# Kernel tuning notes

Hardware: AMD Instinct MI355X
Metric: run time of the kernel (lower is better)

Reference implementation:

```python
import jax, jax.numpy as jnp
import numpy as np

D = 1024      # d_model
HD = 128      # shared k/v head dim == attn_expert_dim
EA = 8        # attention experts
KA = 2        # attention top-k
EF = 16       # ffn experts
KF = 2        # ffn top-k
FH = 512      # ffn expert hidden dim
MAXP = 64     # max relative positions
B, S = 4, 1024
EPS = 1e-5


def setup_inputs() -> dict:
    key = jax.random.key(0)
    ks = jax.random.split(key, 12)
    r = lambda i, shape, scale=0.02: jax.random.normal(ks[i], shape, jnp.float32) * scale
    return {
        "src": jax.random.normal(ks[0], (B, S, D), jnp.float32),
        "ln1_w": jnp.ones((D,), jnp.float32), "ln1_b": jnp.zeros((D,), jnp.float32),
        "ln2_w": jnp.ones((D,), jnp.float32), "ln2_b": jnp.zeros((D,), jnp.float32),
        "attn_gate_w": r(1, (D, EA)),
        "q_w": r(2, (EA, D, HD)), "q_b": jnp.zeros((EA, HD), jnp.float32),
        "k_w": r(3, (D, HD)), "k_b": jnp.zeros((HD,), jnp.float32),
        "v_w": r(4, (D, HD)), "v_b": jnp.zeros((HD,), jnp.float32),
        "o_w": r(5, (EA, HD, D)), "o_b": jnp.zeros((EA, D), jnp.float32),
        "rel_table": r(6, (2 * MAXP + 1, HD)),
        "ff_gate_w": r(7, (D, EF)),
        "ff_w1": r(8, (EF, D, FH)), "ff_b1": jnp.zeros((EF, FH), jnp.float32),
        "ff_w2": r(9, (EF, FH, D)), "ff_b2": jnp.zeros((EF, D), jnp.float32),
    }


def _layer_norm(x, w, b):
    mu = x.mean(-1, keepdims=True)
    var = ((x - mu) ** 2).mean(-1, keepdims=True)
    return (x - mu) * jax.lax.rsqrt(var + EPS) * w + b


def _topk_gates(logits, k):
    # top-k over router logits, softmax over the selected k, scatter to dense [.., E]
    top_vals, top_idx = jax.lax.top_k(logits, k)
    g = jax.nn.softmax(top_vals, axis=-1)
    onehot = jax.nn.one_hot(top_idx, logits.shape[-1], dtype=logits.dtype)  # [...,k,E]
    return jnp.einsum('...k,...ke->...e', g, onehot)


def _moa(x, gate_w, q_w, q_b, k_w, k_b, v_w, v_b, o_w, o_b, rel_table):
    # Mixture-of-attention: per-expert q/out projections, shared k/v, Shaw rel-pos.
    S_ = x.shape[1]
    gates = _topk_gates(x @ gate_w, KA)                                  # [B,S,EA]
    q = (jnp.einsum('bsd,edh->bseh', x, q_w) + q_b) * (HD ** -0.5)       # [B,S,EA,HD]
    k = x @ k_w + k_b                                                    # [B,S,HD]
    v = x @ v_w + v_b
    scores = jnp.einsum('bqeh,bkh->beqk', q, k)                          # [B,EA,S,S]
    rel_s = jnp.einsum('bqeh,rh->beqr', q, rel_table)                    # [B,EA,S,R]
    pos = jnp.arange(S_)
    rel_idx = jnp.clip(pos[None, :] - pos[:, None], -MAXP, MAXP) + MAXP  # [S,S]
    scores = scores + jnp.take_along_axis(rel_s, rel_idx[None, None], axis=-1)
    p = jax.nn.softmax(scores, axis=-1)
    ctx = jnp.einsum('beqk,bkh->bqeh', p, v)                             # [B,S,EA,HD]
    out = jnp.einsum('bqeh,ehd,bqe->bqd', ctx, o_w, gates)
    return out + jnp.einsum('bqe,ed->bqd', gates, o_b)


def _moe_ffn(x, gate_w, w1, b1, w2, b2):
    gates = _topk_gates(x @ gate_w, KF)                                  # [B,S,EF]
    h = jax.nn.relu(jnp.einsum('bsd,edh->bseh', x, w1) + b1)             # [B,S,EF,FH]
    out = jnp.einsum('bseh,ehd,bse->bsd', h, w2, gates)
    return out + jnp.einsum('bse,ed->bsd', gates, b2)


def reference(src, ln1_w, ln1_b, ln2_w, ln2_b, attn_gate_w, q_w, q_b, k_w, k_b,
              v_w, v_b, o_w, o_b, rel_table, ff_gate_w, ff_w1, ff_b1, ff_w2, ff_b2):
    # pre-LN residual block around MoE attention
    res = src
    xn = _layer_norm(src, ln1_w, ln1_b)
    x = res + _moa(xn, attn_gate_w, q_w, q_b, k_w, k_b, v_w, v_b, o_w, o_b, rel_table)
    # pre-LN residual block around MoE FFN
    res = x
    xn = _layer_norm(x, ln2_w, ln2_b)
    return res + _moe_ffn(xn, ff_gate_w, ff_w1, ff_b1, ff_w2, ff_b2)
```

## Files before the change

### kernel.cpp

```cpp
#include <hip/hip_runtime.h>

#define D 1024
#define HD 128
#define EA 8
#define EF 16
#define FH 512
#define MAXPOS 64
#define RNUM 129
#define RSTRIDE 132
#define SEQ 1024
#define NTOK 4096
#define NPAIR (NTOK * 2)
#define NPAD 8320
#define LN_EPS 1e-5f
#define QSCALE 0.08838834764831845f
#define BSTR 40
#define PROW 2048

typedef __attribute__((ext_vector_type(8))) short bf16x8;
typedef __attribute__((ext_vector_type(4))) float f32x4;
typedef __attribute__((ext_vector_type(8))) unsigned short u16x8;

__device__ inline ushort f2b(float f) {
    union { float f; unsigned u; } v; v.f = f;
    unsigned r = (v.u + 0x7fffu + ((v.u >> 16) & 1u)) >> 16;
    return (ushort)r;
}
__device__ inline float b2f(ushort u) {
    union { unsigned u; float f; } v; v.u = (unsigned)u << 16; return v.f;
}
__device__ inline u16x8 cvt8v(float4 a, float4 b) {
    u16x8 r;
    r[0] = f2b(a.x); r[1] = f2b(a.y); r[2] = f2b(a.z); r[3] = f2b(a.w);
    r[4] = f2b(b.x); r[5] = f2b(b.y); r[6] = f2b(b.z); r[7] = f2b(b.w);
    return r;
}

__device__ inline void mfma_step(const short* Asb, const short* Bsb,
                                 int wr, int wc, int m16, int q, f32x4 (&acc)[2][4]) {
    bf16x8 af[2], bfr[4];
#pragma unroll
    for (int i = 0; i < 2; i++) af[i] = *(const bf16x8*)&Asb[(wr + i * 16 + m16) * BSTR + q * 8];
#pragma unroll
    for (int j = 0; j < 4; j++) bfr[j] = *(const bf16x8*)&Bsb[(wc + j * 16 + m16) * BSTR + q * 8];
#pragma unroll
    for (int i = 0; i < 2; i++)
#pragma unroll
        for (int j = 0; j < 4; j++)
            acc[i][j] = __builtin_amdgcn_mfma_f32_16x16x32_bf16(af[i], bfr[j], acc[i][j], 0, 0, 0);
}

__global__ void ln_kernel(const float* __restrict__ x, const float* __restrict__ w,
                          const float* __restrict__ b, float* __restrict__ y) {
    int row = blockIdx.x;
    const float* xr = x + (size_t)row * D;
    float v[4];
    float s = 0.f, s2 = 0.f;
#pragma unroll
    for (int i = 0; i < 4; i++) {
        v[i] = xr[threadIdx.x + i * 256];
        s += v[i]; s2 += v[i] * v[i];
    }
#pragma unroll
    for (int off = 32; off; off >>= 1) { s += __shfl_down(s, off); s2 += __shfl_down(s2, off); }
    __shared__ float red0[4], red1[4];
    int wave = threadIdx.x >> 6, lane = threadIdx.x & 63;
    if (lane == 0) { red0[wave] = s; red1[wave] = s2; }
    __syncthreads();
    float ts = red0[0] + red0[1] + red0[2] + red0[3];
    float ts2 = red1[0] + red1[1] + red1[2] + red1[3];
    float mu = ts * (1.f / D);
    float var = ts2 * (1.f / D) - mu * mu;
    float inv = rsqrtf(var + LN_EPS);
#pragma unroll
    for (int i = 0; i < 4; i++) {
        int d = threadIdx.x + i * 256;
        y[(size_t)row * D + d] = (v[i] - mu) * inv * w[d] + b[d];
    }
}

template <int E>
__global__ void router_kernel(const float* __restrict__ xn, const float* __restrict__ gw,
                              int* __restrict__ idx, float* __restrict__ gate) {
    int t = blockIdx.x;
    int lane = threadIdx.x;
    float acc[E];
#pragma unroll
    for (int e = 0; e < E; e++) acc[e] = 0.f;
    const float* xr = xn + (size_t)t * D;
    for (int d = lane; d < D; d += 64) {
        float xv = xr[d];
#pragma unroll
        for (int e = 0; e < E; e++) acc[e] += xv * gw[d * E + e];
    }
#pragma unroll
    for (int e = 0; e < E; e++) {
#pragma unroll
        for (int off = 32; off; off >>= 1) acc[e] += __shfl_down(acc[e], off);
    }
    if (lane == 0) {
        float v0 = -1e30f, v1 = -1e30f;
        int i0 = 0, i1 = 0;
#pragma unroll
        for (int e = 0; e < E; e++) {
            float a = acc[e];
            if (a > v0) { v1 = v0; i1 = i0; v0 = a; i0 = e; }
            else if (a > v1) { v1 = a; i1 = e; }
        }
        float g0 = 1.f / (1.f + expf(v1 - v0));
        idx[t * 2] = i0; idx[t * 2 + 1] = i1;
        gate[t * 2] = g0; gate[t * 2 + 1] = 1.f - g0;
    }
}

__global__ void abin_zero(int* __restrict__ meta) {
    if (threadIdx.x < 105) meta[threadIdx.x] = 0;
}
__global__ void abin_count(const int* __restrict__ aidx, int* __restrict__ meta) {
    int i = blockIdx.x * 256 + threadIdx.x;
    if (i < NPAIR) {
        int e = aidx[i];
        int b = (i >> 1) >> 10;
        atomicAdd(&meta[e * 4 + b], 1);
    }
}
__global__ void abin_scan(int* __restrict__ meta) {
    if (threadIdx.x == 0 && blockIdx.x == 0) {
        int s = 0;
        for (int bin = 0; bin < 32; bin++) {
            if ((bin & 3) == 0) meta[96 + (bin >> 2)] = s;
            meta[32 + bin] = s; meta[64 + bin] = s; s += meta[bin];
        }
        meta[96 + 8] = s;
    }
}
__global__ void abin_scatter(const int* __restrict__ aidx, int* __restrict__ meta,
                             int* __restrict__ list, int* __restrict__ inv) {
    int i = blockIdx.x * 256 + threadIdx.x;
    if (i < NPAIR) {
        int e = aidx[i];
        int b = (i >> 1) >> 10;
        int pos = atomicAdd(&meta[64 + e * 4 + b], 1);
        list[pos] = i;
        inv[i] = pos;
    }
}

__global__ void bin_zero(int* __restrict__ meta) {
    if (threadIdx.x < 48) meta[threadIdx.x] = 0;
}
__global__ void bin_count(const int* __restrict__ fidx, int* __restrict__ meta) {
    int i = blockIdx.x * 256 + threadIdx.x;
    if (i < NPAIR) atomicAdd(&meta[fidx[i]], 1);
}
__global__ void bin_scan(int* __restrict__ meta) {
    if (threadIdx.x == 0 && blockIdx.x == 0) {
        int s = 0;
        for (int e = 0; e < EF; e++) { meta[16 + e] = s; meta[32 + e] = s; s += meta[e]; }
    }
}
__global__ void bin_scatter(const int* __restrict__ fidx, int* __restrict__ meta,
                            int* __restrict__ list, int* __restrict__ inv) {
    int i = blockIdx.x * 256 + threadIdx.x;
    if (i < NPAIR) {
        int e = fidx[i];
        int pos = atomicAdd(&meta[32 + e], 1);
        list[pos] = i;
        inv[i] = pos;
    }
}

template <int R, int C>
__global__ void convT_kernel(const float* __restrict__ in, ushort* __restrict__ out) {
    int e = blockIdx.z;
    int r0 = blockIdx.x * 32, c0 = blockIdx.y * 32;
    __shared__ float tile[32][33];
    int tx = threadIdx.x & 31, ty = threadIdx.x >> 5;
    const float* src = in + (size_t)e * R * C;
#pragma unroll
    for (int i = 0; i < 32; i += 8)
        tile[ty + i][tx] = src[(size_t)(r0 + ty + i) * C + c0 + tx];
    __syncthreads();
    ushort* dst = out + (size_t)e * C * R;
#pragma unroll
    for (int i = 0; i < 32; i += 8)
        dst[(size_t)(c0 + ty + i) * R + r0 + tx] = f2b(tile[tx][ty + i]);
}

__global__ void conv_kernel(const float* __restrict__ in, ushort* __restrict__ out, int n) {
    int i = blockIdx.x * 256 + threadIdx.x;
    if (i < n) out[i] = f2b(in[i]);
}

__global__ __launch_bounds__(256) void kv_mfma(
    const float* __restrict__ xn, const ushort* __restrict__ kwt,
    const ushort* __restrict__ vwt, float* __restrict__ kpart, float* __restrict__ vpart) {
    const ushort* W = blockIdx.z ? vwt : kwt;
    float* outp = blockIdx.z ? vpart : kpart;
    int m0 = blockIdx.x * 64;
    int s = blockIdx.y;
    int kbase = s * 256;
    __shared__ __align__(16) short As[2][64 * BSTR];
    __shared__ __align__(16) short Bs[2][128 * BSTR];
    int tid = threadIdx.x, aRow = tid >> 2, aOff = (tid & 3) * 8;
    const float* ap = xn + (size_t)(m0 + aRow) * D + kbase + aOff;
    const ushort* bp0 = W + (size_t)aRow * D + kbase + aOff;
    const ushort* bp1 = bp0 + (size_t)64 * D;
    int w = tid >> 6, lid = tid & 63;
    int wr = (w >> 1) * 32, wc = (w & 1) * 64;
    int m16 = lid & 15, q = lid >> 4;
    f32x4 acc[2][4] = {};
    float4 ra0 = *(const float4*)ap, ra1 = *(const float4*)(ap + 4);
    u16x8 rb0 = *(const u16x8*)bp0, rb1 = *(const u16x8*)bp1;
    *(u16x8*)&As[0][aRow * BSTR + aOff] = cvt8v(ra0, ra1);
    *(u16x8*)&Bs[0][aRow * BSTR + aOff] = rb0;
    *(u16x8*)&Bs[0][(aRow + 64) * BSTR + aOff] = rb1;
    __syncthreads();
    int cur = 0;
    for (int k = 1; k < 8; k++) {
        ra0 = *(const float4*)(ap + k * 32); ra1 = *(const float4*)(ap + k * 32 + 4);
        rb0 = *(const u16x8*)(bp0 + k * 32); rb1 = *(const u16x8*)(bp1 + k * 32);
        mfma_step(As[cur], Bs[cur], wr, wc, m16, q, acc);
        int nxt = cur ^ 1;
        *(u16x8*)&As[nxt][aRow * BSTR + aOff] = cvt8v(ra0, ra1);
        *(u16x8*)&Bs[nxt][aRow * BSTR + aOff] = rb0;
        *(u16x8*)&Bs[nxt][(aRow + 64) * BSTR + aOff] = rb1;
        __syncthreads();
        cur = nxt;
    }
    mfma_step(As[cur], Bs[cur], wr, wc, m16, q, acc);
#pragma unroll
    for (int i = 0; i < 2; i++)
#pragma unroll
        for (int r = 0; r < 4; r++) {
            int m = m0 + wr + i * 16 + q * 4 + r;
#pragma unroll
            for (int j = 0; j < 4; j++)
                outp[((size_t)s * NTOK + m) * HD + wc + j * 16 + m16] = acc[i][j][r];
        }
}

__global__ void kv_reduce(const float* __restrict__ kpart, const float* __restrict__ vpart,
                          const float* __restrict__ kb, const float* __restrict__ vb,
                          float* __restrict__ kbf, float* __restrict__ vbf) {
    int t = blockIdx.x, h = threadIdx.x;
    float ka = kb[h], va = vb[h];
#pragma unroll
    for (int s = 0; s < 4; s++) {
        ka += kpart[((size_t)s * NTOK + t) * HD + h];
        va += vpart[((size_t)s * NTOK + t) * HD + h];
    }
    kbf[(size_t)t * HD + h] = ka;
    vbf[(size_t)t * HD + h] = va;
}

__global__ __launch_bounds__(256) void q_mfma(
    const float* __restrict__ xn, const ushort* __restrict__ qwt,
    const int* __restrict__ meta, const int* __restrict__ list, float* __restrict__ qpart) {
    int e = blockIdx.z;
    int o = meta[96 + e], c = meta[97 + e] - o;
    int m0 = blockIdx.x * 64;
    if (m0 >= c) return;
    int s = blockIdx.y;
    int kbase = s * 256;
    __shared__ __align__(16) short As[2][64 * BSTR];
    __shared__ __align__(16) short Bs[2][128 * BSTR];
    int tid = threadIdx.x, aRow = tid >> 2, aOff = (tid & 3) * 8;
    int ri = o + m0 + aRow; if (ri > NPAIR - 1) ri = NPAIR - 1;
    const float* ap = xn + (size_t)(list[ri] >> 1) * D + kbase + aOff;
    const ushort* bp0 = qwt + (size_t)e * HD * D + (size_t)aRow * D + kbase + aOff;
    const ushort* bp1 = bp0 + (size_t)64 * D;
    int w = tid >> 6, lid = tid & 63;
    int wr = (w >> 1) * 32, wc = (w & 1) * 64;
    int m16 = lid & 15, q = lid >> 4;
    f32x4 acc[2][4] = {};
    float4 ra0 = *(const float4*)ap, ra1 = *(const float4*)(ap + 4);
    u16x8 rb0 = *(const u16x8*)bp0, rb1 = *(const u16x8*)bp1;
    *(u16x8*)&As[0][aRow * BSTR + aOff] = cvt8v(ra0, ra1);
    *(u16x8*)&Bs[0][aRow * BSTR + aOff] = rb0;
    *(u16x8*)&Bs[0][(aRow + 64) * BSTR + aOff] = rb1;
    __syncthreads();
    int cur = 0;
    for (int k = 1; k < 8; k++) {
        ra0 = *(const float4*)(ap + k * 32); ra1 = *(const float4*)(ap + k * 32 + 4);
        rb0 = *(const u16x8*)(bp0 + k * 32); rb1 = *(const u16x8*)(bp1 + k * 32);
        mfma_step(As[cur], Bs[cur], wr, wc, m16, q, acc);
        int nxt = cur ^ 1;
        *(u16x8*)&As[nxt][aRow * BSTR + aOff] = cvt8v(ra0, ra1);
        *(u16x8*)&Bs[nxt][aRow * BSTR + aOff] = rb0;
        *(u16x8*)&Bs[nxt][(aRow + 64) * BSTR + aOff] = rb1;
        __syncthreads();
        cur = nxt;
    }
    mfma_step(As[cur], Bs[cur], wr, wc, m16, q, acc);
#pragma unroll
    for (int i = 0; i < 2; i++)
#pragma unroll
        for (int r = 0; r < 4; r++) {
            int pos = o + m0 + wr + i * 16 + q * 4 + r;
            if (pos < o + c) {
#pragma unroll
                for (int j = 0; j < 4; j++)
                    qpart[((size_t)s * NPAD + pos) * HD + wc + j * 16 + m16] = acc[i][j][r];
            }
        }
}

__global__ void q_reduce(const float* __restrict__ qpart, const float* __restrict__ qb,
                         const int* __restrict__ aidx, const int* __restrict__ list,
                         ushort* __restrict__ Qg) {
    int pos = blockIdx.x, h = threadIdx.x;
    int e = aidx[list[pos]];
    float a = qb[e * HD + h];
#pragma unroll
    for (int s = 0; s < 4; s++) a += qpart[((size_t)s * NPAD + pos) * HD + h];
    Qg[(size_t)pos * HD + h] = f2b(a * QSCALE);
}

__global__ __launch_bounds__(256) void rel_mfma(
    const ushort* __restrict__ Qg, const ushort* __restrict__ relb,
    float* __restrict__ R) {
    int m0 = blockIdx.x * 64;
    int n0 = blockIdx.y * 128;
    __shared__ __align__(16) short As[2][64 * BSTR];
    __shared__ __align__(16) short Bs[2][128 * BSTR];
    int tid = threadIdx.x, aRow = tid >> 2, aOff = (tid & 3) * 8;
    const ushort* ap = Qg + (size_t)(m0 + aRow) * HD + aOff;
    int br0 = n0 + aRow;      if (br0 > RNUM - 1) br0 = RNUM - 1;
    int br1 = n0 + aRow + 64; if (br1 > RNUM - 1) br1 = RNUM - 1;
    const ushort* bp0 = relb + (size_t)br0 * HD + aOff;
    const ushort* bp1 = relb + (size_t)br1 * HD + aOff;
    int w = tid >> 6, lid = tid & 63;
    int wr = (w >> 1) * 32, wc = (w & 1) * 64;
    int m16 = lid & 15, q = lid >> 4;
    f32x4 acc[2][4] = {};
    u16x8 ra = *(const u16x8*)ap;
    u16x8 rb0 = *(const u16x8*)bp0, rb1 = *(const u16x8*)bp1;
    *(u16x8*)&As[0][aRow * BSTR + aOff] = ra;
    *(u16x8*)&Bs[0][aRow * BSTR + aOff] = rb0;
    *(u16x8*)&Bs[0][(aRow + 64) * BSTR + aOff] = rb1;
    __syncthreads();
    int cur = 0;
    for (int k = 1; k < 4; k++) {
        ra = *(const u16x8*)(ap + k * 32);
        rb0 = *(const u16x8*)(bp0 + k * 32); rb1 = *(const u16x8*)(bp1 + k * 32);
        mfma_step(As[cur], Bs[cur], wr, wc, m16, q, acc);
        int nxt = cur ^ 1;
        *(u16x8*)&As[nxt][aRow * BSTR + aOff] = ra;
        *(u16x8*)&Bs[nxt][aRow * BSTR + aOff] = rb0;
        *(u16x8*)&Bs[nxt][(aRow + 64) * BSTR + aOff] = rb1;
        __syncthreads();
        cur = nxt;
    }
    mfma_step(As[cur], Bs[cur], wr, wc, m16, q, acc);
#pragma unroll
    for (int i = 0; i < 2; i++)
#pragma unroll
        for (int r = 0; r < 4; r++) {
            int pos = m0 + wr + i * 16 + q * 4 + r;
#pragma unroll
            for (int j = 0; j < 4; j++) {
                int n = n0 + wc + j * 16 + m16;
                if (n < RNUM) R[(size_t)pos * RSTRIDE + n] = acc[i][j][r];
            }
        }
}

__global__ __launch_bounds__(256) void s_mfma(
    const ushort* __restrict__ Qg, const float* __restrict__ kbf,
    const float* __restrict__ R, const int* __restrict__ meta,
    const int* __restrict__ list, float* __restrict__ S) {
    int bin = blockIdx.z;
    int o = meta[32 + bin], c = meta[bin];
    int m0 = blockIdx.x * 64;
    if (m0 >= c) return;
    int b = bin & 3;
    int n0 = blockIdx.y * 128;
    __shared__ __align__(16) short As[2][64 * BSTR];
    __shared__ __align__(16) short Bs[2][128 * BSTR];
    int tid = threadIdx.x, aRow = tid >> 2, aOff = (tid & 3) * 8;
    const ushort* ap = Qg + (size_t)(o + m0 + aRow) * HD + aOff;
    const float* bp0 = kbf + (size_t)b * SEQ * HD + (size_t)(n0 + aRow) * HD + aOff;
    const float* bp1 = bp0 + (size_t)64 * HD;
    int w = tid >> 6, lid = tid & 63;
    int wr = (w >> 1) * 32, wc = (w & 1) * 64;
    int m16 = lid & 15, q = lid >> 4;
    f32x4 acc[2][4] = {};
    u16x8 ra = *(const u16x8*)ap;
    float4 rb0a = *(const float4*)bp0, rb0b = *(const float4*)(bp0 + 4);
    float4 rb1a = *(const float4*)bp1, rb1b = *(const float4*)(bp1 + 4);
    *(u16x8*)&As[0][aRow * BSTR + aOff] = ra;
    *(u16x8*)&Bs[0][aRow * BSTR + aOff] = cvt8v(rb0a, rb0b);
    *(u16x8*)&Bs[0][(aRow + 64) * BSTR + aOff] = cvt8v(rb1a, rb1b);
    __syncthreads();
    int cur = 0;
    for (int k = 1; k < 4; k++) {
        ra = *(const u16x8*)(ap + k * 32);
        rb0a = *(const float4*)(bp0 + k * 32); rb0b = *(const float4*)(bp0 + k * 32 + 4);
        rb1a = *(const float4*)(bp1 + k * 32); rb1b = *(const float4*)(bp1 + k * 32 + 4);
        mfma_step(As[cur], Bs[cur], wr, wc, m16, q, acc);
        int nxt = cur ^ 1;
        *(u16x8*)&As[nxt][aRow * BSTR + aOff] = ra;
        *(u16x8*)&Bs[nxt][aRow * BSTR + aOff] = cvt8v(rb0a, rb0b);
        *(u16x8*)&Bs[nxt][(aRow + 64) * BSTR + aOff] = cvt8v(rb1a, rb1b);
        __syncthreads();
        cur = nxt;
    }
    mfma_step(As[cur], Bs[cur], wr, wc, m16, q, acc);
#pragma unroll
    for (int i = 0; i < 2; i++)
#pragma unroll
        for (int r = 0; r < 4; r++) {
            int pos = o + m0 + wr + i * 16 + q * 4 + r;
            if (pos < o + c) {
                int qpos = (list[pos] >> 1) & (SEQ - 1);
                const float* Rrow = R + (size_t)pos * RSTRIDE;
                float* sr = S + (size_t)pos * SEQ;
#pragma unroll
                for (int j = 0; j < 4; j++) {
                    int key = n0 + wc + j * 16 + m16;
                    int rix = key - qpos;
                    rix = (rix < -MAXPOS ? -MAXPOS : (rix > MAXPOS ? MAXPOS : rix)) + MAXPOS;
                    sr[key] = acc[i][j][r] + Rrow[rix];
                }
            }
        }
}

__global__ __launch_bounds__(256) void softmax_kernel(float* __restrict__ S) {
    int row = blockIdx.x;
    float4* sr = (float4*)(S + (size_t)row * SEQ);
    float4 v = sr[threadIdx.x];
    float m = fmaxf(fmaxf(v.x, v.y), fmaxf(v.z, v.w));
#pragma unroll
    for (int off = 32; off; off >>= 1) m = fmaxf(m, __shfl_down(m, off));
    __shared__ float red0[4], red1[4];
    int wave = threadIdx.x >> 6, lane = threadIdx.x & 63;
    if (lane == 0) red0[wave] = m;
    __syncthreads();
    m = fmaxf(fmaxf(red0[0], red0[1]), fmaxf(red0[2], red0[3]));
    v.x = __expf(v.x - m); v.y = __expf(v.y - m);
    v.z = __expf(v.z - m); v.w = __expf(v.w - m);
    float s = v.x + v.y + v.z + v.w;
#pragma unroll
    for (int off = 32; off; off >>= 1) s += __shfl_down(s, off);
    if (lane == 0) red1[wave] = s;
    __syncthreads();
    float inv = 1.f / (red1[0] + red1[1] + red1[2] + red1[3]);
    ushort* pr = (ushort*)(S + (size_t)row * SEQ);
    ushort4 p4 = { f2b(v.x * inv), f2b(v.y * inv), f2b(v.z * inv), f2b(v.w * inv) };
    *(ushort4*)(pr + threadIdx.x * 4) = p4;
}

__global__ __launch_bounds__(256) void pv_mfma(
    const ushort* __restrict__ Pb, const ushort* __restrict__ vt16,
    const int* __restrict__ meta, float* __restrict__ ppart) {
    int bin = blockIdx.z;
    int o = meta[32 + bin], c = meta[bin];
    int m0 = blockIdx.x * 64;
    if (m0 >= c) return;
    int b = bin & 3;
    int s = blockIdx.y;
    int kbase = s * 256;
    __shared__ __align__(16) short As[2][64 * BSTR];
    __shared__ __align__(16) short Bs[2][128 * BSTR];
    int tid = threadIdx.x, aRow = tid >> 2, aOff = (tid & 3) * 8;
    const ushort* ap = Pb + (size_t)(o + m0 + aRow) * PROW + kbase + aOff;
    const ushort* bp0 = vt16 + (size_t)b * HD * SEQ + (size_t)aRow * SEQ + kbase + aOff;
    const ushort* bp1 = bp0 + (size_t)64 * SEQ;
    int w = tid >> 6, lid = tid & 63;
    int wr = (w >> 1) * 32, wc = (w & 1) * 64;
    int m16 = lid & 15, q = lid >> 4;
    f32x4 acc[2][4] = {};
    u16x8 ra = *(const u16x8*)ap;
    u16x8 rb0 = *(const u16x8*)bp0, rb1 = *(const u16x8*)bp1;
    *(u16x8*)&As[0][aRow * BSTR + aOff] = ra;
    *(u16x8*)&Bs[0][aRow * BSTR + aOff] = rb0;
    *(u16x8*)&Bs[0][(aRow + 64) * BSTR + aOff] = rb1;
    __syncthreads();
    int cur = 0;
    for (int k = 1; k < 8; k++) {
        ra = *(const u16x8*)(ap + k * 32);
        rb0 = *(const u16x8*)(bp0 + k * 32); rb1 = *(const u16x8*)(bp1 + k * 32);
        mfma_step(As[cur], Bs[cur], wr, wc, m16, q, acc);
        int nxt = cur ^ 1;
        *(u16x8*)&As[nxt][aRow * BSTR + aOff] = ra;
        *(u16x8*)&Bs[nxt][aRow * BSTR + aOff] = rb0;
        *(u16x8*)&Bs[nxt][(aRow + 64) * BSTR + aOff] = rb1;
        __syncthreads();
        cur = nxt;
    }
    mfma_step(As[cur], Bs[cur], wr, wc, m16, q, acc);
#pragma unroll
    for (int i = 0; i < 2; i++)
#pragma unroll
        for (int r = 0; r < 4; r++) {
            int pos = o + m0 + wr + i * 16 + q * 4 + r;
            if (pos < o + c) {
#pragma unroll
                for (int j = 0; j < 4; j++)
                    ppart[((size_t)s * NPAD + pos) * HD + wc + j * 16 + m16] = acc[i][j][r];
            }
        }
}

__global__ void pv_reduce(const float* __restrict__ ppart, const float* __restrict__ aga,
                          const int* __restrict__ list, float* __restrict__ ctxf) {
    int pos = blockIdx.x, h = threadIdx.x;
    float g = aga[list[pos]];
    float a = 0.f;
#pragma unroll
    for (int s = 0; s < 4; s++) a += ppart[((size_t)s * NPAD + pos) * HD + h];
    ctxf[(size_t)pos * HD + h] = a * g;
}

__global__ __launch_bounds__(256) void o_mfma(
    const float* __restrict__ ctxf, const ushort* __restrict__ owt,
    const int* __restrict__ meta, ushort* __restrict__ Ofb) {
    int e = blockIdx.z;
    int o = meta[96 + e], c = meta[97 + e] - o;
    int m0 = blockIdx.x * 64;
    if (m0 >= c) return;
    int n0 = blockIdx.y * 128;
    __shared__ __align__(16) short As[2][64 * BSTR];
    __shared__ __align__(16) short Bs[2][128 * BSTR];
    int tid = threadIdx.x, aRow = tid >> 2, aOff = (tid & 3) * 8;
    const float* ap = ctxf + (size_t)(o + m0 + aRow) * HD + aOff;
    const ushort* bp0 = owt + (size_t)e * D * HD + (size_t)(n0 + aRow) * HD + aOff;
    const ushort* bp1 = bp0 + (size_t)64 * HD;
    int w = tid >> 6, lid = tid & 63;
    int wr = (w >> 1) * 32, wc = (w & 1) * 64;
    int m16 = lid & 15, q = lid >> 4;
    f32x4 acc[2][4] = {};
    float4 ra0 = *(const float4*)ap, ra1 = *(const float4*)(ap + 4);
    u16x8 rb0 = *(const u16x8*)bp0, rb1 = *(const u16x8*)bp1;
    *(u16x8*)&As[0][aRow * BSTR + aOff] = cvt8v(ra0, ra1);
    *(u16x8*)&Bs[0][aRow * BSTR + aOff] = rb0;
    *(u16x8*)&Bs[0][(aRow + 64) * BSTR + aOff] = rb1;
    __syncthreads();
    int cur = 0;
    for (int k = 1; k < 4; k++) {
        ra0 = *(const float4*)(ap + k * 32); ra1 = *(const float4*)(ap + k * 32 + 4);
        rb0 = *(const u16x8*)(bp0 + k * 32); rb1 = *(const u16x8*)(bp1 + k * 32);
        mfma_step(As[cur], Bs[cur], wr, wc, m16, q, acc);
        int nxt = cur ^ 1;
        *(u16x8*)&As[nxt][aRow * BSTR + aOff] = cvt8v(ra0, ra1);
        *(u16x8*)&Bs[nxt][aRow * BSTR + aOff] = rb0;
        *(u16x8*)&Bs[nxt][(aRow + 64) * BSTR + aOff] = rb1;
        __syncthreads();
        cur = nxt;
    }
    mfma_step(As[cur], Bs[cur], wr, wc, m16, q, acc);
#pragma unroll
    for (int i = 0; i < 2; i++)
#pragma unroll
        for (int r = 0; r < 4; r++) {
            int pos = o + m0 + wr + i * 16 + q * 4 + r;
            if (pos < o + c) {
#pragma unroll
                for (int j = 0; j < 4; j++)
                    Ofb[(size_t)pos * D + n0 + wc + j * 16 + m16] = f2b(acc[i][j][r]);
            }
        }
}

__global__ void attn_combine(const float* __restrict__ src, const float* __restrict__ ob,
                             const int* __restrict__ aidx, const float* __restrict__ aga,
                             const int* __restrict__ ainv, const ushort* __restrict__ Ofb,
                             float* __restrict__ x1) {
    int t = blockIdx.x, tid = threadIdx.x;
    int e0 = aidx[t * 2], e1 = aidx[t * 2 + 1];
    float g0 = aga[t * 2], g1 = aga[t * 2 + 1];
    int p0 = ainv[t * 2], p1 = ainv[t * 2 + 1];
#pragma unroll
    for (int i = 0; i < 4; i++) {
        int d = tid + i * 256;
        x1[(size_t)t * D + d] = src[(size_t)t * D + d]
                              + g0 * ob[e0 * D + d] + g1 * ob[e1 * D + d]
                              + b2f(Ofb[(size_t)p0 * D + d]) + b2f(Ofb[(size_t)p1 * D + d]);
    }
}

__global__ __launch_bounds__(256) void ffn_mfma1(
    const float* __restrict__ xn2, const ushort* __restrict__ w1t,
    const float* __restrict__ b1, const int* __restrict__ meta,
    const int* __restrict__ list, const float* __restrict__ fga,
    ushort* __restrict__ Hb) {
    int e = blockIdx.z;
    int o = meta[16 + e], c = meta[e];
    int m0 = blockIdx.x * 64;
    if (m0 >= c) return;
    int n0 = blockIdx.y * 128;
    __shared__ __align__(16) short As[2][64 * BSTR];
    __shared__ __align__(16) short Bs[2][128 * BSTR];
    int tid = threadIdx.x, aRow = tid >> 2, aOff = (tid & 3) * 8;
    int ri = o + m0 + aRow; if (ri > NPAIR - 1) ri = NPAIR - 1;
    const float* ap = xn2 + (size_t)(list[ri] >> 1) * D + aOff;
    const ushort* bp0 = w1t + ((size_t)e * FH + n0 + aRow) * D + aOff;
    const ushort* bp1 = bp0 + (size_t)64 * D;
    int w = tid >> 6, lid = tid & 63;
    int wr = (w >> 1) * 32, wc = (w & 1) * 64;
    int m16 = lid & 15, q = lid >> 4;
    f32x4 acc[2][4] = {};
    float4 ra0 = *(const float4*)ap, ra1 = *(const float4*)(ap + 4);
    u16x8 rb0 = *(const u16x8*)bp0, rb1 = *(const u16x8*)bp1;
    *(u16x8*)&As[0][aRow * BSTR + aOff] = cvt8v(ra0, ra1);
    *(u16x8*)&Bs[0][aRow * BSTR + aOff] = rb0;
    *(u16x8*)&Bs[0][(aRow + 64) * BSTR + aOff] = rb1;
    __syncthreads();
    int cur = 0;
    for (int k = 1; k < 32; k++) {
        ra0 = *(const float4*)(ap + k * 32); ra1 = *(const float4*)(ap + k * 32 + 4);
        rb0 = *(const u16x8*)(bp0 + k * 32); rb1 = *(const u16x8*)(bp1 + k * 32);
        mfma_step(As[cur], Bs[cur], wr, wc, m16, q, acc);
        int nxt = cur ^ 1;
        *(u16x8*)&As[nxt][aRow * BSTR + aOff] = cvt8v(ra0, ra1);
        *(u16x8*)&Bs[nxt][aRow * BSTR + aOff] = rb0;
        *(u16x8*)&Bs[nxt][(aRow + 64) * BSTR + aOff] = rb1;
        __syncthreads();
        cur = nxt;
    }
    mfma_step(As[cur], Bs[cur], wr, wc, m16, q, acc);
#pragma unroll
    for (int i = 0; i < 2; i++)
#pragma unroll
        for (int r = 0; r < 4; r++) {
            int pos = o + m0 + wr + i * 16 + q * 4 + r;
            if (pos < o + c) {
                float g = fga[list[pos]];
#pragma unroll
                for (int j = 0; j < 4; j++) {
                    int n = n0 + wc + j * 16 + m16;
                    Hb[(size_t)pos * FH + n] = f2b(g * fmaxf(acc[i][j][r] + b1[e * FH + n], 0.f));
                }
            }
        }
}

__global__ __launch_bounds__(256) void ffn_mfma2(
    const ushort* __restrict__ Hb, const ushort* __restrict__ w2t,
    const int* __restrict__ meta, ushort* __restrict__ Of2b) {
    int e = blockIdx.z;
    int o = meta[16 + e], c = meta[e];
    int m0 = blockIdx.x * 64;
    if (m0 >= c) return;
    int n0 = blockIdx.y * 128;
    __shared__ __align__(16) short As[2][64 * BSTR];
    __shared__ __align__(16) short Bs[2][128 * BSTR];
    int tid = threadIdx.x, aRow = tid >> 2, aOff = (tid & 3) * 8;
    const ushort* ap = Hb + (size_t)(o + m0 + aRow) * FH + aOff;
    const ushort* bp0 = w2t + ((size_t)e * D + n0 + aRow) * FH + aOff;
    const ushort* bp1 = bp0 + (size_t)64 * FH;
    int w = tid >> 6, lid = tid & 63;
    int wr = (w >> 1) * 32, wc = (w & 1) * 64;
    int m16 = lid & 15, q = lid >> 4;
    f32x4 acc[2][4] = {};
    u16x8 ra = *(const u16x8*)ap;
    u16x8 rb0 = *(const u16x8*)bp0, rb1 = *(const u16x8*)bp1;
    *(u16x8*)&As[0][aRow * BSTR + aOff] = ra;
    *(u16x8*)&Bs[0][aRow * BSTR + aOff] = rb0;
    *(u16x8*)&Bs[0][(aRow + 64) * BSTR + aOff] = rb1;
    __syncthreads();
    int cur = 0;
    for (int k = 1; k < 16; k++) {
        ra = *(const u16x8*)(ap + k * 32);
        rb0 = *(const u16x8*)(bp0 + k * 32); rb1 = *(const u16x8*)(bp1 + k * 32);
        mfma_step(As[cur], Bs[cur], wr, wc, m16, q, acc);
        int nxt = cur ^ 1;
        *(u16x8*)&As[nxt][aRow * BSTR + aOff] = ra;
        *(u16x8*)&Bs[nxt][aRow * BSTR + aOff] = rb0;
        *(u16x8*)&Bs[nxt][(aRow + 64) * BSTR + aOff] = rb1;
        __syncthreads();
        cur = nxt;
    }
    mfma_step(As[cur], Bs[cur], wr, wc, m16, q, acc);
#pragma unroll
    for (int i = 0; i < 2; i++)
#pragma unroll
        for (int r = 0; r < 4; r++) {
            int pos = o + m0 + wr + i * 16 + q * 4 + r;
            if (pos < o + c) {
#pragma unroll
                for (int j = 0; j < 4; j++)
                    Of2b[(size_t)pos * D + n0 + wc + j * 16 + m16] = f2b(acc[i][j][r]);
            }
        }
}

__global__ void ffn_combine(const float* __restrict__ x1, const float* __restrict__ b2,
                            const int* __restrict__ fidx, const float* __restrict__ fga,
                            const int* __restrict__ finv, const ushort* __restrict__ Of2b,
                            float* __restrict__ out) {
    int t = blockIdx.x, tid = threadIdx.x;
    int e0 = fidx[t * 2], e1 = fidx[t * 2 + 1];
    float g0 = fga[t * 2], g1 = fga[t * 2 + 1];
    int p0 = finv[t * 2], p1 = finv[t * 2 + 1];
#pragma unroll
    for (int i = 0; i < 4; i++) {
        int d = tid + i * 256;
        out[(size_t)t * D + d] = x1[(size_t)t * D + d]
                               + g0 * b2[e0 * D + d] + g1 * b2[e1 * D + d]
                               + b2f(Of2b[(size_t)p0 * D + d]) + b2f(Of2b[(size_t)p1 * D + d]);
    }
}

extern "C" void kernel_launch(void* const* d_in, const int* in_sizes, int n_in,
                              void* d_out, int out_size, void* d_ws, size_t ws_size,
                              hipStream_t stream) {
    const float* src   = (const float*)d_in[0];
    const float* ln1_w = (const float*)d_in[1];
    const float* ln1_b = (const float*)d_in[2];
    const float* ln2_w = (const float*)d_in[3];
    const float* ln2_b = (const float*)d_in[4];
    const float* agw   = (const float*)d_in[5];
    const float* qw    = (const float*)d_in[6];
    const float* qb    = (const float*)d_in[7];
    const float* kw    = (const float*)d_in[8];
    const float* kb    = (const float*)d_in[9];
    const float* vw    = (const float*)d_in[10];
    const float* vb    = (const float*)d_in[11];
    const float* ow    = (const float*)d_in[12];
    const float* ob    = (const float*)d_in[13];
    const float* rel   = (const float*)d_in[14];
    const float* fgw   = (const float*)d_in[15];
    const float* w1    = (const float*)d_in[16];
    const float* b1    = (const float*)d_in[17];
    const float* w2    = (const float*)d_in[18];
    const float* b2    = (const float*)d_in[19];
    float* out = (float*)d_out;

    char* p = (char*)d_ws;
    float* xn1  = (float*)p; p += (size_t)NTOK * D * 4;
    float* x1   = (float*)p; p += (size_t)NTOK * D * 4;
    char*  sreg = p;         p += (size_t)NPAD * SEQ * 4;
    float*  Sbuf = (float*)sreg;
    ushort* Pb   = (ushort*)sreg;
    ushort* Ofb  = (ushort*)sreg;
    ushort* w1t  = (ushort*)sreg;
    ushort* w2t  = (ushort*)(sreg + (size_t)16777216);
    char*  reg  = p;         p += (size_t)NPAD * 128 * 6 + (size_t)NPAIR * RSTRIDE * 4;
    float*  ctxf = (float*)reg;
    ushort* Qg   = (ushort*)(reg + (size_t)NPAD * 128 * 4);
    float*  Rbuf = (float*)(reg + (size_t)NPAD * 128 * 6);
    ushort* Hb   = (ushort*)reg;
    char*  arena = p;        p += (size_t)4 * NPAD * 128 * 4;
    float*  kpart = (float*)arena;
    float*  vpart = (float*)(arena + (size_t)4 * NTOK * HD * 4);
    float*  qpart = (float*)arena;
    float*  ppart = (float*)arena;
    ushort* Of2b  = (ushort*)arena;
    float* kbf  = (float*)p; p += (size_t)NTOK * HD * 4;
    float* vbf  = (float*)p; p += (size_t)NTOK * HD * 4;
    ushort* vt16 = (ushort*)p; p += (size_t)NTOK * HD * 2;
    ushort* kwt = (ushort*)p; p += (size_t)HD * D * 2;
    ushort* vwt = (ushort*)p; p += (size_t)HD * D * 2;
    ushort* qwt = (ushort*)p; p += (size_t)EA * HD * D * 2;
    ushort* owt = (ushort*)p; p += (size_t)EA * D * HD * 2;
    ushort* relb = (ushort*)p; p += (size_t)RNUM * HD * 2 + 256;
    int*   aidx = (int*)p;   p += NPAIR * 4;
    float* aga  = (float*)p; p += NPAIR * 4;
    int*   fidx = (int*)p;   p += NPAIR * 4;
    float* fga  = (float*)p; p += NPAIR * 4;
    int*   ameta = (int*)p;  p += 128 * 4;
    int*   alist = (int*)p;  p += NPAIR * 4;
    int*   ainv = (int*)p;   p += NPAIR * 4;
    int*   fmeta = (int*)p;  p += 64 * 4;
    int*   flist = (int*)p;  p += NPAIR * 4;
    int*   finv = (int*)p;   p += NPAIR * 4;
    float* xn2 = xn1;

    ln_kernel<<<NTOK, 256, 0, stream>>>(src, ln1_w, ln1_b, xn1);
    router_kernel<EA><<<NTOK, 64, 0, stream>>>(xn1, agw, aidx, aga);
    abin_zero<<<1, 128, 0, stream>>>(ameta);
    abin_count<<<NPAIR / 256, 256, 0, stream>>>(aidx, ameta);
    abin_scan<<<1, 64, 0, stream>>>(ameta);
    abin_scatter<<<NPAIR / 256, 256, 0, stream>>>(aidx, ameta, alist, ainv);
    convT_kernel<1024, 128><<<dim3(32, 4, 1), 256, 0, stream>>>(kw, kwt);
    convT_kernel<1024, 128><<<dim3(32, 4, 1), 256, 0, stream>>>(vw, vwt);
    convT_kernel<1024, 128><<<dim3(32, 4, EA), 256, 0, stream>>>(qw, qwt);
    convT_kernel<128, 1024><<<dim3(4, 32, EA), 256, 0, stream>>>(ow, owt);
    conv_kernel<<<(RNUM * HD + 255) / 256, 256, 0, stream>>>(rel, relb, RNUM * HD);
    kv_mfma<<<dim3(64, 4, 2), 256, 0, stream>>>(xn1, kwt, vwt, kpart, vpart);
    kv_reduce<<<NTOK, 128, 0, stream>>>(kpart, vpart, kb, vb, kbf, vbf);
    convT_kernel<1024, 128><<<dim3(32, 4, 4), 256, 0, stream>>>(vbf, vt16);
    q_mfma<<<dim3(40, 4, EA), 256, 0, stream>>>(xn1, qwt, ameta, alist, qpart);
    q_reduce<<<NPAIR, 128, 0, stream>>>(qpart, qb, aidx, alist, Qg);
    rel_mfma<<<dim3(NPAIR / 64, 2), 256, 0, stream>>>(Qg, relb, Rbuf);
    s_mfma<<<dim3(12, 8, 32), 256, 0, stream>>>(Qg, kbf, Rbuf, ameta, alist, Sbuf);
    softmax_kernel<<<NPAIR, 256, 0, stream>>>(Sbuf);
    pv_mfma<<<dim3(12, 4, 32), 256, 0, stream>>>(Pb, vt16, ameta, ppart);
    pv_reduce<<<NPAIR, 128, 0, stream>>>(ppart, aga, alist, ctxf);
    o_mfma<<<dim3(40, 8, EA), 256, 0, stream>>>(ctxf, owt, ameta, Ofb);
    attn_combine<<<NTOK, 256, 0, stream>>>(src, ob, aidx, aga, ainv, Ofb, x1);

    ln_kernel<<<NTOK, 256, 0, stream>>>(x1, ln2_w, ln2_b, xn2);
    router_kernel<EF><<<NTOK, 64, 0, stream>>>(xn2, fgw, fidx, fga);
    bin_zero<<<1, 64, 0, stream>>>(fmeta);
    bin_count<<<NPAIR / 256, 256, 0, stream>>>(fidx, fmeta);
    bin_scan<<<1, 64, 0, stream>>>(fmeta);
    bin_scatter<<<NPAIR / 256, 256, 0, stream>>>(fidx, fmeta, flist, finv);
    convT_kernel<1024, 512><<<dim3(32, 16, EF), 256, 0, stream>>>(w1, w1t);
    convT_kernel<512, 1024><<<dim3(16, 32, EF), 256, 0, stream>>>(w2, w2t);
    ffn_mfma1<<<dim3(20, 4, EF), 256, 0, stream>>>(xn2, w1t, b1, fmeta, flist, fga, Hb);
    ffn_mfma2<<<dim3(20, 8, EF), 256, 0, stream>>>(Hb, w2t, fmeta, Of2b);
    ffn_combine<<<NTOK, 256, 0, stream>>>(x1, b2, fidx, fga, finv, Of2b, out);
}
```

Baseline: 516.8 us.

## Stage GEMM tiles with global_load_lds and feed bf16 activations from producers

```diff
diff --git a/kernel.cpp b/kernel.cpp
--- a/kernel.cpp
+++ b/kernel.cpp
@@ -14,7 +14,7 @@
 #define NPAD 8320
 #define LN_EPS 1e-5f
 #define QSCALE 0.08838834764831845f
-#define BSTR 40
+#define BSTR 32
 #define PROW 2048
 
 typedef __attribute__((ext_vector_type(8))) short bf16x8;
@@ -29,11 +29,10 @@
 __device__ inline float b2f(ushort u) {
     union { unsigned u; float f; } v; v.u = (unsigned)u << 16; return v.f;
 }
-__device__ inline u16x8 cvt8v(float4 a, float4 b) {
-    u16x8 r;
-    r[0] = f2b(a.x); r[1] = f2b(a.y); r[2] = f2b(a.z); r[3] = f2b(a.w);
-    r[4] = f2b(b.x); r[5] = f2b(b.y); r[6] = f2b(b.z); r[7] = f2b(b.w);
-    return r;
+
+__device__ __forceinline__ void gll(const void* g, void* l) {
+    __builtin_amdgcn_global_load_lds((const __attribute__((address_space(1))) void*)g,
+                                     (__attribute__((address_space(3))) void*)l, 16, 0, 0);
 }
 
 __device__ inline void mfma_step(const short* Asb, const short* Bsb,
@@ -51,7 +50,8 @@
 }
 
 __global__ void ln_kernel(const float* __restrict__ x, const float* __restrict__ w,
-                          const float* __restrict__ b, float* __restrict__ y) {
+                          const float* __restrict__ b, float* __restrict__ y,
+                          ushort* __restrict__ yb) {
     int row = blockIdx.x;
     const float* xr = x + (size_t)row * D;
     float v[4];
@@ -75,7 +75,9 @@
 #pragma unroll
     for (int i = 0; i < 4; i++) {
         int d = threadIdx.x + i * 256;
-        y[(size_t)row * D + d] = (v[i] - mu) * inv * w[d] + b[d];
+        float o = (v[i] - mu) * inv * w[d] + b[d];
+        y[(size_t)row * D + d] = o;
+        yb[(size_t)row * D + d] = f2b(o);
     }
 }
 
@@ -192,8 +194,9 @@
     if (i < n) out[i] = f2b(in[i]);
 }
 
+
 __global__ __launch_bounds__(256) void kv_mfma(
-    const float* __restrict__ xn, const ushort* __restrict__ kwt,
+    const ushort* __restrict__ xnb, const ushort* __restrict__ kwt,
     const ushort* __restrict__ vwt, float* __restrict__ kpart, float* __restrict__ vpart) {
     const ushort* W = blockIdx.z ? vwt : kwt;
     float* outp = blockIdx.z ? vpart : kpart;
@@ -202,29 +205,23 @@
     int kbase = s * 256;
     __shared__ __align__(16) short As[2][64 * BSTR];
     __shared__ __align__(16) short Bs[2][128 * BSTR];
-    int tid = threadIdx.x, aRow = tid >> 2, aOff = (tid & 3) * 8;
-    const float* ap = xn + (size_t)(m0 + aRow) * D + kbase + aOff;
-    const ushort* bp0 = W + (size_t)aRow * D + kbase + aOff;
-    const ushort* bp1 = bp0 + (size_t)64 * D;
-    int w = tid >> 6, lid = tid & 63;
+    int tid = threadIdx.x, w = tid >> 6, lane = tid & 63;
+    int sr = lane >> 2, sc = (lane & 3) * 8;
+    const ushort* ap = xnb + (size_t)(m0 + w * 16 + sr) * D + kbase + sc;
+    const ushort* bp0 = W + (size_t)(w * 32 + sr) * D + kbase + sc;
+    const ushort* bp1 = bp0 + (size_t)16 * D;
     int wr = (w >> 1) * 32, wc = (w & 1) * 64;
-    int m16 = lid & 15, q = lid >> 4;
+    int m16 = lane & 15, q = lane >> 4;
     f32x4 acc[2][4] = {};
-    float4 ra0 = *(const float4*)ap, ra1 = *(const float4*)(ap + 4);
-    u16x8 rb0 = *(const u16x8*)bp0, rb1 = *(const u16x8*)bp1;
-    *(u16x8*)&As[0][aRow * BSTR + aOff] = cvt8v(ra0, ra1);
-    *(u16x8*)&Bs[0][aRow * BSTR + aOff] = rb0;
-    *(u16x8*)&Bs[0][(aRow + 64) * BSTR + aOff] = rb1;
+    gll(ap, &As[0][w * 512]); gll(bp0, &Bs[0][w * 1024]); gll(bp1, &Bs[0][w * 1024 + 512]);
     __syncthreads();
     int cur = 0;
     for (int k = 1; k < 8; k++) {
-        ra0 = *(const float4*)(ap + k * 32); ra1 = *(const float4*)(ap + k * 32 + 4);
-        rb0 = *(const u16x8*)(bp0 + k * 32); rb1 = *(const u16x8*)(bp1 + k * 32);
+        int nxt = cur ^ 1;
+        gll(ap + k * 32, &As[nxt][w * 512]);
+        gll(bp0 + k * 32, &Bs[nxt][w * 1024]);
+        gll(bp1 + k * 32, &Bs[nxt][w * 1024 + 512]);
         mfma_step(As[cur], Bs[cur], wr, wc, m16, q, acc);
-        int nxt = cur ^ 1;
-        *(u16x8*)&As[nxt][aRow * BSTR + aOff] = cvt8v(ra0, ra1);
-        *(u16x8*)&Bs[nxt][aRow * BSTR + aOff] = rb0;
-        *(u16x8*)&Bs[nxt][(aRow + 64) * BSTR + aOff] = rb1;
         __syncthreads();
         cur = nxt;
     }
@@ -242,7 +239,7 @@
 
 __global__ void kv_reduce(const float* __restrict__ kpart, const float* __restrict__ vpart,
                           const float* __restrict__ kb, const float* __restrict__ vb,
-                          float* __restrict__ kbf, float* __restrict__ vbf) {
+                          ushort* __restrict__ kb16, float* __restrict__ vbf) {
     int t = blockIdx.x, h = threadIdx.x;
     float ka = kb[h], va = vb[h];
 #pragma unroll
@@ -250,12 +247,12 @@
         ka += kpart[((size_t)s * NTOK + t) * HD + h];
         va += vpart[((size_t)s * NTOK + t) * HD + h];
     }
-    kbf[(size_t)t * HD + h] = ka;
+    kb16[(size_t)t * HD + h] = f2b(ka);
     vbf[(size_t)t * HD + h] = va;
 }
 
 __global__ __launch_bounds__(256) void q_mfma(
-    const float* __restrict__ xn, const ushort* __restrict__ qwt,
+    const ushort* __restrict__ xnb, const ushort* __restrict__ qwt,
     const int* __restrict__ meta, const int* __restrict__ list, float* __restrict__ qpart) {
     int e = blockIdx.z;
     int o = meta[96 + e], c = meta[97 + e] - o;
@@ -265,30 +262,24 @@
     int kbase = s * 256;
     __shared__ __align__(16) short As[2][64 * BSTR];
     __shared__ __align__(16) short Bs[2][128 * BSTR];
-    int tid = threadIdx.x, aRow = tid >> 2, aOff = (tid & 3) * 8;
-    int ri = o + m0 + aRow; if (ri > NPAIR - 1) ri = NPAIR - 1;
-    const float* ap = xn + (size_t)(list[ri] >> 1) * D + kbase + aOff;
-    const ushort* bp0 = qwt + (size_t)e * HD * D + (size_t)aRow * D + kbase + aOff;
-    const ushort* bp1 = bp0 + (size_t)64 * D;
-    int w = tid >> 6, lid = tid & 63;
+    int tid = threadIdx.x, w = tid >> 6, lane = tid & 63;
+    int sr = lane >> 2, sc = (lane & 3) * 8;
+    int ri = o + m0 + w * 16 + sr; if (ri > NPAIR - 1) ri = NPAIR - 1;
+    const ushort* ap = xnb + (size_t)(list[ri] >> 1) * D + kbase + sc;
+    const ushort* bp0 = qwt + (size_t)e * HD * D + (size_t)(w * 32 + sr) * D + kbase + sc;
+    const ushort* bp1 = bp0 + (size_t)16 * D;
     int wr = (w >> 1) * 32, wc = (w & 1) * 64;
-    int m16 = lid & 15, q = lid >> 4;
+    int m16 = lane & 15, q = lane >> 4;
     f32x4 acc[2][4] = {};
-    float4 ra0 = *(const float4*)ap, ra1 = *(const float4*)(ap + 4);
-    u16x8 rb0 = *(const u16x8*)bp0, rb1 = *(const u16x8*)bp1;
-    *(u16x8*)&As[0][aRow * BSTR + aOff] = cvt8v(ra0, ra1);
-    *(u16x8*)&Bs[0][aRow * BSTR + aOff] = rb0;
-    *(u16x8*)&Bs[0][(aRow + 64) * BSTR + aOff] = rb1;
+    gll(ap, &As[0][w * 512]); gll(bp0, &Bs[0][w * 1024]); gll(bp1, &Bs[0][w * 1024 + 512]);
     __syncthreads();
     int cur = 0;
     for (int k = 1; k < 8; k++) {
-        ra0 = *(const float4*)(ap + k * 32); ra1 = *(const float4*)(ap + k * 32 + 4);
-        rb0 = *(const u16x8*)(bp0 + k * 32); rb1 = *(const u16x8*)(bp1 + k * 32);
+        int nxt = cur ^ 1;
+        gll(ap + k * 32, &As[nxt][w * 512]);
+        gll(bp0 + k * 32, &Bs[nxt][w * 1024]);
+        gll(bp1 + k * 32, &Bs[nxt][w * 1024 + 512]);
         mfma_step(As[cur], Bs[cur], wr, wc, m16, q, acc);
-        int nxt = cur ^ 1;
-        *(u16x8*)&As[nxt][aRow * BSTR + aOff] = cvt8v(ra0, ra1);
-        *(u16x8*)&Bs[nxt][aRow * BSTR + aOff] = rb0;
-        *(u16x8*)&Bs[nxt][(aRow + 64) * BSTR + aOff] = rb1;
         __syncthreads();
         cur = nxt;
     }
@@ -324,31 +315,25 @@
     int n0 = blockIdx.y * 128;
     __shared__ __align__(16) short As[2][64 * BSTR];
     __shared__ __align__(16) short Bs[2][128 * BSTR];
-    int tid = threadIdx.x, aRow = tid >> 2, aOff = (tid & 3) * 8;
-    const ushort* ap = Qg + (size_t)(m0 + aRow) * HD + aOff;
-    int br0 = n0 + aRow;      if (br0 > RNUM - 1) br0 = RNUM - 1;
-    int br1 = n0 + aRow + 64; if (br1 > RNUM - 1) br1 = RNUM - 1;
-    const ushort* bp0 = relb + (size_t)br0 * HD + aOff;
-    const ushort* bp1 = relb + (size_t)br1 * HD + aOff;
-    int w = tid >> 6, lid = tid & 63;
+    int tid = threadIdx.x, w = tid >> 6, lane = tid & 63;
+    int sr = lane >> 2, sc = (lane & 3) * 8;
+    const ushort* ap = Qg + (size_t)(m0 + w * 16 + sr) * HD + sc;
+    int r0 = n0 + w * 32 + sr;      if (r0 > RNUM - 1) r0 = RNUM - 1;
+    int r1 = n0 + w * 32 + 16 + sr; if (r1 > RNUM - 1) r1 = RNUM - 1;
+    const ushort* bp0 = relb + (size_t)r0 * HD + sc;
+    const ushort* bp1 = relb + (size_t)r1 * HD + sc;
     int wr = (w >> 1) * 32, wc = (w & 1) * 64;
-    int m16 = lid & 15, q = lid >> 4;
+    int m16 = lane & 15, q = lane >> 4;
     f32x4 acc[2][4] = {};
-    u16x8 ra = *(const u16x8*)ap;
-    u16x8 rb0 = *(const u16x8*)bp0, rb1 = *(const u16x8*)bp1;
-    *(u16x8*)&As[0][aRow * BSTR + aOff] = ra;
-    *(u16x8*)&Bs[0][aRow * BSTR + aOff] = rb0;
-    *(u16x8*)&Bs[0][(aRow + 64) * BSTR + aOff] = rb1;
+    gll(ap, &As[0][w * 512]); gll(bp0, &Bs[0][w * 1024]); gll(bp1, &Bs[0][w * 1024 + 512]);
     __syncthreads();
     int cur = 0;
     for (int k = 1; k < 4; k++) {
-        ra = *(const u16x8*)(ap + k * 32);
-        rb0 = *(const u16x8*)(bp0 + k * 32); rb1 = *(const u16x8*)(bp1 + k * 32);
+        int nxt = cur ^ 1;
+        gll(ap + k * 32, &As[nxt][w * 512]);
+        gll(bp0 + k * 32, &Bs[nxt][w * 1024]);
+        gll(bp1 + k * 32, &Bs[nxt][w * 1024 + 512]);
         mfma_step(As[cur], Bs[cur], wr, wc, m16, q, acc);
-        int nxt = cur ^ 1;
-        *(u16x8*)&As[nxt][aRow * BSTR + aOff] = ra;
-        *(u16x8*)&Bs[nxt][aRow * BSTR + aOff] = rb0;
-        *(u16x8*)&Bs[nxt][(aRow + 64) * BSTR + aOff] = rb1;
         __syncthreads();
         cur = nxt;
     }
@@ -367,7 +352,7 @@
 }
 
 __global__ __launch_bounds__(256) void s_mfma(
-    const ushort* __restrict__ Qg, const float* __restrict__ kbf,
+    const ushort* __restrict__ Qg, const ushort* __restrict__ kb16,
     const float* __restrict__ R, const int* __restrict__ meta,
     const int* __restrict__ list, float* __restrict__ S) {
     int bin = blockIdx.z;
@@ -378,31 +363,23 @@
     int n0 = blockIdx.y * 128;
     __shared__ __align__(16) short As[2][64 * BSTR];
     __shared__ __align__(16) short Bs[2][128 * BSTR];
-    int tid = threadIdx.x, aRow = tid >> 2, aOff = (tid & 3) * 8;
-    const ushort* ap = Qg + (size_t)(o + m0 + aRow) * HD + aOff;
-    const float* bp0 = kbf + (size_t)b * SEQ * HD + (size_t)(n0 + aRow) * HD + aOff;
-    const float* bp1 = bp0 + (size_t)64 * HD;
-    int w = tid >> 6, lid = tid & 63;
+    int tid = threadIdx.x, w = tid >> 6, lane = tid & 63;
+    int sr = lane >> 2, sc = (lane & 3) * 8;
+    const ushort* ap = Qg + (size_t)(o + m0 + w * 16 + sr) * HD + sc;
+    const ushort* bp0 = kb16 + (size_t)b * SEQ * HD + (size_t)(n0 + w * 32 + sr) * HD + sc;
+    const ushort* bp1 = bp0 + (size_t)16 * HD;
     int wr = (w >> 1) * 32, wc = (w & 1) * 64;
-    int m16 = lid & 15, q = lid >> 4;
+    int m16 = lane & 15, q = lane >> 4;
     f32x4 acc[2][4] = {};
-    u16x8 ra = *(const u16x8*)ap;
-    float4 rb0a = *(const float4*)bp0, rb0b = *(const float4*)(bp0 + 4);
-    float4 rb1a = *(const float4*)bp1, rb1b = *(const float4*)(bp1 + 4);
-    *(u16x8*)&As[0][aRow * BSTR + aOff] = ra;
-    *(u16x8*)&Bs[0][aRow * BSTR + aOff] = cvt8v(rb0a, rb0b);
-    *(u16x8*)&Bs[0][(aRow + 64) * BSTR + aOff] = cvt8v(rb1a, rb1b);
+    gll(ap, &As[0][w * 512]); gll(bp0, &Bs[0][w * 1024]); gll(bp1, &Bs[0][w * 1024 + 512]);
     __syncthreads();
     int cur = 0;
     for (int k = 1; k < 4; k++) {
-        ra = *(const u16x8*)(ap + k * 32);
-        rb0a = *(const float4*)(bp0 + k * 32); rb0b = *(const float4*)(bp0 + k * 32 + 4);
-        rb1a = *(const float4*)(bp1 + k * 32); rb1b = *(const float4*)(bp1 + k * 32 + 4);
+        int nxt = cur ^ 1;
+        gll(ap + k * 32, &As[nxt][w * 512]);
+        gll(bp0 + k * 32, &Bs[nxt][w * 1024]);
+        gll(bp1 + k * 32, &Bs[nxt][w * 1024 + 512]);
         mfma_step(As[cur], Bs[cur], wr, wc, m16, q, acc);
-        int nxt = cur ^ 1;
-        *(u16x8*)&As[nxt][aRow * BSTR + aOff] = ra;
-        *(u16x8*)&Bs[nxt][aRow * BSTR + aOff] = cvt8v(rb0a, rb0b);
-        *(u16x8*)&Bs[nxt][(aRow + 64) * BSTR + aOff] = cvt8v(rb1a, rb1b);
         __syncthreads();
         cur = nxt;
     }
@@ -415,13 +392,13 @@
             if (pos < o + c) {
                 int qpos = (list[pos] >> 1) & (SEQ - 1);
                 const float* Rrow = R + (size_t)pos * RSTRIDE;
-                float* sr = S + (size_t)pos * SEQ;
+                float* sr_ = S + (size_t)pos * SEQ;
 #pragma unroll
                 for (int j = 0; j < 4; j++) {
                     int key = n0 + wc + j * 16 + m16;
                     int rix = key - qpos;
                     rix = (rix < -MAXPOS ? -MAXPOS : (rix > MAXPOS ? MAXPOS : rix)) + MAXPOS;
-                    sr[key] = acc[i][j][r] + Rrow[rix];
+                    sr_[key] = acc[i][j][r] + Rrow[rix];
                 }
             }
         }
@@ -464,29 +441,23 @@
     int kbase = s * 256;
     __shared__ __align__(16) short As[2][64 * BSTR];
     __shared__ __align__(16) short Bs[2][128 * BSTR];
-    int tid = threadIdx.x, aRow = tid >> 2, aOff = (tid & 3) * 8;
-    const ushort* ap = Pb + (size_t)(o + m0 + aRow) * PROW + kbase + aOff;
-    const ushort* bp0 = vt16 + (size_t)b * HD * SEQ + (size_t)aRow * SEQ + kbase + aOff;
-    const ushort* bp1 = bp0 + (size_t)64 * SEQ;
-    int w = tid >> 6, lid = tid & 63;
+    int tid = threadIdx.x, w = tid >> 6, lane = tid & 63;
+    int sr = lane >> 2, sc = (lane & 3) * 8;
+    const ushort* ap = Pb + (size_t)(o + m0 + w * 16 + sr) * PROW + kbase + sc;
+    const ushort* bp0 = vt16 + (size_t)b * HD * SEQ + (size_t)(w * 32 + sr) * SEQ + kbase + sc;
+    const ushort* bp1 = bp0 + (size_t)16 * SEQ;
     int wr = (w >> 1) * 32, wc = (w & 1) * 64;
-    int m16 = lid & 15, q = lid >> 4;
+    int m16 = lane & 15, q = lane >> 4;
     f32x4 acc[2][4] = {};
-    u16x8 ra = *(const u16x8*)ap;
-    u16x8 rb0 = *(const u16x8*)bp0, rb1 = *(const u16x8*)bp1;
-    *(u16x8*)&As[0][aRow * BSTR + aOff] = ra;
-    *(u16x8*)&Bs[0][aRow * BSTR + aOff] = rb0;
-    *(u16x8*)&Bs[0][(aRow + 64) * BSTR + aOff] = rb1;
+    gll(ap, &As[0][w * 512]); gll(bp0, &Bs[0][w * 1024]); gll(bp1, &Bs[0][w * 1024 + 512]);
     __syncthreads();
     int cur = 0;
     for (int k = 1; k < 8; k++) {
-        ra = *(const u16x8*)(ap + k * 32);
-        rb0 = *(const u16x8*)(bp0 + k * 32); rb1 = *(const u16x8*)(bp1 + k * 32);
+        int nxt = cur ^ 1;
+        gll(ap + k * 32, &As[nxt][w * 512]);
+        gll(bp0 + k * 32, &Bs[nxt][w * 1024]);
+        gll(bp1 + k * 32, &Bs[nxt][w * 1024 + 512]);
         mfma_step(As[cur], Bs[cur], wr, wc, m16, q, acc);
-        int nxt = cur ^ 1;
-        *(u16x8*)&As[nxt][aRow * BSTR + aOff] = ra;
-        *(u16x8*)&Bs[nxt][aRow * BSTR + aOff] = rb0;
-        *(u16x8*)&Bs[nxt][(aRow + 64) * BSTR + aOff] = rb1;
         __syncthreads();
         cur = nxt;
     }
@@ -505,17 +476,17 @@
 }
 
 __global__ void pv_reduce(const float* __restrict__ ppart, const float* __restrict__ aga,
-                          const int* __restrict__ list, float* __restrict__ ctxf) {
+                          const int* __restrict__ list, ushort* __restrict__ ctx16) {
     int pos = blockIdx.x, h = threadIdx.x;
     float g = aga[list[pos]];
     float a = 0.f;
 #pragma unroll
     for (int s = 0; s < 4; s++) a += ppart[((size_t)s * NPAD + pos) * HD + h];
-    ctxf[(size_t)pos * HD + h] = a * g;
+    ctx16[(size_t)pos * HD + h] = f2b(a * g);
 }
 
 __global__ __launch_bounds__(256) void o_mfma(
-    const float* __restrict__ ctxf, const ushort* __restrict__ owt,
+    const ushort* __restrict__ ctx16, const ushort* __restrict__ owt,
     const int* __restrict__ meta, ushort* __restrict__ Ofb) {
     int e = blockIdx.z;
     int o = meta[96 + e], c = meta[97 + e] - o;
@@ -524,29 +495,23 @@
     int n0 = blockIdx.y * 128;
     __shared__ __align__(16) short As[2][64 * BSTR];
     __shared__ __align__(16) short Bs[2][128 * BSTR];
-    int tid = threadIdx.x, aRow = tid >> 2, aOff = (tid & 3) * 8;
-    const float* ap = ctxf + (size_t)(o + m0 + aRow) * HD + aOff;
-    const ushort* bp0 = owt + (size_t)e * D * HD + (size_t)(n0 + aRow) * HD + aOff;
-    const ushort* bp1 = bp0 + (size_t)64 * HD;
-    int w = tid >> 6, lid = tid & 63;
+    int tid = threadIdx.x, w = tid >> 6, lane = tid & 63;
+    int sr = lane >> 2, sc = (lane & 3) * 8;
+    const ushort* ap = ctx16 + (size_t)(o + m0 + w * 16 + sr) * HD + sc;
+    const ushort* bp0 = owt + (size_t)e * D * HD + (size_t)(n0 + w * 32 + sr) * HD + sc;
+    const ushort* bp1 = bp0 + (size_t)16 * HD;
     int wr = (w >> 1) * 32, wc = (w & 1) * 64;
-    int m16 = lid & 15, q = lid >> 4;
+    int m16 = lane & 15, q = lane >> 4;
     f32x4 acc[2][4] = {};
-    float4 ra0 = *(const float4*)ap, ra1 = *(const float4*)(ap + 4);
-    u16x8 rb0 = *(const u16x8*)bp0, rb1 = *(const u16x8*)bp1;
-    *(u16x8*)&As[0][aRow * BSTR + aOff] = cvt8v(ra0, ra1);
-    *(u16x8*)&Bs[0][aRow * BSTR + aOff] = rb0;
-    *(u16x8*)&Bs[0][(aRow + 64) * BSTR + aOff] = rb1;
+    gll(ap, &As[0][w * 512]); gll(bp0, &Bs[0][w * 1024]); gll(bp1, &Bs[0][w * 1024 + 512]);
     __syncthreads();
     int cur = 0;
     for (int k = 1; k < 4; k++) {
-        ra0 = *(const float4*)(ap + k * 32); ra1 = *(const float4*)(ap + k * 32 + 4);
-        rb0 = *(const u16x8*)(bp0 + k * 32); rb1 = *(const u16x8*)(bp1 + k * 32);
+        int nxt = cur ^ 1;
+        gll(ap + k * 32, &As[nxt][w * 512]);
+        gll(bp0 + k * 32, &Bs[nxt][w * 1024]);
+        gll(bp1 + k * 32, &Bs[nxt][w * 1024 + 512]);
         mfma_step(As[cur], Bs[cur], wr, wc, m16, q, acc);
-        int nxt = cur ^ 1;
-        *(u16x8*)&As[nxt][aRow * BSTR + aOff] = cvt8v(ra0, ra1);
-        *(u16x8*)&Bs[nxt][aRow * BSTR + aOff] = rb0;
-        *(u16x8*)&Bs[nxt][(aRow + 64) * BSTR + aOff] = rb1;
         __syncthreads();
         cur = nxt;
     }
@@ -582,7 +547,7 @@
 }
 
 __global__ __launch_bounds__(256) void ffn_mfma1(
-    const float* __restrict__ xn2, const ushort* __restrict__ w1t,
+    const ushort* __restrict__ xnb2, const ushort* __restrict__ w1t,
     const float* __restrict__ b1, const int* __restrict__ meta,
     const int* __restrict__ list, const float* __restrict__ fga,
     ushort* __restrict__ Hb) {
@@ -593,30 +558,24 @@
     int n0 = blockIdx.y * 128;
     __shared__ __align__(16) short As[2][64 * BSTR];
     __shared__ __align__(16) short Bs[2][128 * BSTR];
-    int tid = threadIdx.x, aRow = tid >> 2, aOff = (tid & 3) * 8;
-    int ri = o + m0 + aRow; if (ri > NPAIR - 1) ri = NPAIR - 1;
-    const float* ap = xn2 + (size_t)(list[ri] >> 1) * D + aOff;
-    const ushort* bp0 = w1t + ((size_t)e * FH + n0 + aRow) * D + aOff;
-    const ushort* bp1 = bp0 + (size_t)64 * D;
-    int w = tid >> 6, lid = tid & 63;
+    int tid = threadIdx.x, w = tid >> 6, lane = tid & 63;
+    int sr = lane >> 2, sc = (lane & 3) * 8;
+    int ri = o + m0 + w * 16 + sr; if (ri > NPAIR - 1) ri = NPAIR - 1;
+    const ushort* ap = xnb2 + (size_t)(list[ri] >> 1) * D + sc;
+    const ushort* bp0 = w1t + ((size_t)e * FH + n0 + w * 32 + sr) * D + sc;
+    const ushort* bp1 = bp0 + (size_t)16 * D;
     int wr = (w >> 1) * 32, wc = (w & 1) * 64;
-    int m16 = lid & 15, q = lid >> 4;
+    int m16 = lane & 15, q = lane >> 4;
     f32x4 acc[2][4] = {};
-    float4 ra0 = *(const float4*)ap, ra1 = *(const float4*)(ap + 4);
-    u16x8 rb0 = *(const u16x8*)bp0, rb1 = *(const u16x8*)bp1;
-    *(u16x8*)&As[0][aRow * BSTR + aOff] = cvt8v(ra0, ra1);
-    *(u16x8*)&Bs[0][aRow * BSTR + aOff] = rb0;
-    *(u16x8*)&Bs[0][(aRow + 64) * BSTR + aOff] = rb1;
+    gll(ap, &As[0][w * 512]); gll(bp0, &Bs[0][w * 1024]); gll(bp1, &Bs[0][w * 1024 + 512]);
     __syncthreads();
     int cur = 0;
     for (int k = 1; k < 32; k++) {
-        ra0 = *(const float4*)(ap + k * 32); ra1 = *(const float4*)(ap + k * 32 + 4);
-        rb0 = *(const u16x8*)(bp0 + k * 32); rb1 = *(const u16x8*)(bp1 + k * 32);
+        int nxt = cur ^ 1;
+        gll(ap + k * 32, &As[nxt][w * 512]);
+        gll(bp0 + k * 32, &Bs[nxt][w * 1024]);
+        gll(bp1 + k * 32, &Bs[nxt][w * 1024 + 512]);
         mfma_step(As[cur], Bs[cur], wr, wc, m16, q, acc);
-        int nxt = cur ^ 1;
-        *(u16x8*)&As[nxt][aRow * BSTR + aOff] = cvt8v(ra0, ra1);
-        *(u16x8*)&Bs[nxt][aRow * BSTR + aOff] = rb0;
-        *(u16x8*)&Bs[nxt][(aRow + 64) * BSTR + aOff] = rb1;
         __syncthreads();
         cur = nxt;
     }
@@ -647,29 +606,23 @@
     int n0 = blockIdx.y * 128;
     __shared__ __align__(16) short As[2][64 * BSTR];
     __shared__ __align__(16) short Bs[2][128 * BSTR];
-    int tid = threadIdx.x, aRow = tid >> 2, aOff = (tid & 3) * 8;
-    const ushort* ap = Hb + (size_t)(o + m0 + aRow) * FH + aOff;
-    const ushort* bp0 = w2t + ((size_t)e * D + n0 + aRow) * FH + aOff;
-    const ushort* bp1 = bp0 + (size_t)64 * FH;
-    int w = tid >> 6, lid = tid & 63;
+    int tid = threadIdx.x, w = tid >> 6, lane = tid & 63;
+    int sr = lane >> 2, sc = (lane & 3) * 8;
+    const ushort* ap = Hb + (size_t)(o + m0 + w * 16 + sr) * FH + sc;
+    const ushort* bp0 = w2t + ((size_t)e * D + n0 + w * 32 + sr) * FH + sc;
+    const ushort* bp1 = bp0 + (size_t)16 * FH;
     int wr = (w >> 1) * 32, wc = (w & 1) * 64;
-    int m16 = lid & 15, q = lid >> 4;
+    int m16 = lane & 15, q = lane >> 4;
     f32x4 acc[2][4] = {};
-    u16x8 ra = *(const u16x8*)ap;
-    u16x8 rb0 = *(const u16x8*)bp0, rb1 = *(const u16x8*)bp1;
-    *(u16x8*)&As[0][aRow * BSTR + aOff] = ra;
-    *(u16x8*)&Bs[0][aRow * BSTR + aOff] = rb0;
-    *(u16x8*)&Bs[0][(aRow + 64) * BSTR + aOff] = rb1;
+    gll(ap, &As[0][w * 512]); gll(bp0, &Bs[0][w * 1024]); gll(bp1, &Bs[0][w * 1024 + 512]);
     __syncthreads();
     int cur = 0;
     for (int k = 1; k < 16; k++) {
-        ra = *(const u16x8*)(ap + k * 32);
-        rb0 = *(const u16x8*)(bp0 + k * 32); rb1 = *(const u16x8*)(bp1 + k * 32);
+        int nxt = cur ^ 1;
+        gll(ap + k * 32, &As[nxt][w * 512]);
+        gll(bp0 + k * 32, &Bs[nxt][w * 1024]);
+        gll(bp1 + k * 32, &Bs[nxt][w * 1024 + 512]);
         mfma_step(As[cur], Bs[cur], wr, wc, m16, q, acc);
-        int nxt = cur ^ 1;
-        *(u16x8*)&As[nxt][aRow * BSTR + aOff] = ra;
-        *(u16x8*)&Bs[nxt][aRow * BSTR + aOff] = rb0;
-        *(u16x8*)&Bs[nxt][(aRow + 64) * BSTR + aOff] = rb1;
         __syncthreads();
         cur = nxt;
     }
@@ -739,7 +692,7 @@
     ushort* w1t  = (ushort*)sreg;
     ushort* w2t  = (ushort*)(sreg + (size_t)16777216);
     char*  reg  = p;         p += (size_t)NPAD * 128 * 6 + (size_t)NPAIR * RSTRIDE * 4;
-    float*  ctxf = (float*)reg;
+    ushort* ctx16 = (ushort*)reg;
     ushort* Qg   = (ushort*)(reg + (size_t)NPAD * 128 * 4);
     float*  Rbuf = (float*)(reg + (size_t)NPAD * 128 * 6);
     ushort* Hb   = (ushort*)reg;
@@ -749,7 +702,7 @@
     float*  qpart = (float*)arena;
     float*  ppart = (float*)arena;
     ushort* Of2b  = (ushort*)arena;
-    float* kbf  = (float*)p; p += (size_t)NTOK * HD * 4;
+    ushort* kb16 = (ushort*)p; p += (size_t)NTOK * HD * 2;
     float* vbf  = (float*)p; p += (size_t)NTOK * HD * 4;
     ushort* vt16 = (ushort*)p; p += (size_t)NTOK * HD * 2;
     ushort* kwt = (ushort*)p; p += (size_t)HD * D * 2;
@@ -767,9 +720,10 @@
     int*   fmeta = (int*)p;  p += 64 * 4;
     int*   flist = (int*)p;  p += NPAIR * 4;
     int*   finv = (int*)p;   p += NPAIR * 4;
+    ushort* xnb = (ushort*)p; p += (size_t)NTOK * D * 2;
     float* xn2 = xn1;
 
-    ln_kernel<<<NTOK, 256, 0, stream>>>(src, ln1_w, ln1_b, xn1);
+    ln_kernel<<<NTOK, 256, 0, stream>>>(src, ln1_w, ln1_b, xn1, xnb);
     router_kernel<EA><<<NTOK, 64, 0, stream>>>(xn1, agw, aidx, aga);
     abin_zero<<<1, 128, 0, stream>>>(ameta);
     abin_count<<<NPAIR / 256, 256, 0, stream>>>(aidx, ameta);
@@ -780,20 +734,20 @@
     convT_kernel<1024, 128><<<dim3(32, 4, EA), 256, 0, stream>>>(qw, qwt);
     convT_kernel<128, 1024><<<dim3(4, 32, EA), 256, 0, stream>>>(ow, owt);
     conv_kernel<<<(RNUM * HD + 255) / 256, 256, 0, stream>>>(rel, relb, RNUM * HD);
-    kv_mfma<<<dim3(64, 4, 2), 256, 0, stream>>>(xn1, kwt, vwt, kpart, vpart);
-    kv_reduce<<<NTOK, 128, 0, stream>>>(kpart, vpart, kb, vb, kbf, vbf);
+    kv_mfma<<<dim3(64, 4, 2), 256, 0, stream>>>(xnb, kwt, vwt, kpart, vpart);
+    kv_reduce<<<NTOK, 128, 0, stream>>>(kpart, vpart, kb, vb, kb16, vbf);
     convT_kernel<1024, 128><<<dim3(32, 4, 4), 256, 0, stream>>>(vbf, vt16);
-    q_mfma<<<dim3(40, 4, EA), 256, 0, stream>>>(xn1, qwt, ameta, alist, qpart);
+    q_mfma<<<dim3(40, 4, EA), 256, 0, stream>>>(xnb, qwt, ameta, alist, qpart);
     q_reduce<<<NPAIR, 128, 0, stream>>>(qpart, qb, aidx, alist, Qg);
     rel_mfma<<<dim3(NPAIR / 64, 2), 256, 0, stream>>>(Qg, relb, Rbuf);
-    s_mfma<<<dim3(12, 8, 32), 256, 0, stream>>>(Qg, kbf, Rbuf, ameta, alist, Sbuf);
+    s_mfma<<<dim3(12, 8, 32), 256, 0, stream>>>(Qg, kb16, Rbuf, ameta, alist, Sbuf);
     softmax_kernel<<<NPAIR, 256, 0, stream>>>(Sbuf);
     pv_mfma<<<dim3(12, 4, 32), 256, 0, stream>>>(Pb, vt16, ameta, ppart);
-    pv_reduce<<<NPAIR, 128, 0, stream>>>(ppart, aga, alist, ctxf);
-    o_mfma<<<dim3(40, 8, EA), 256, 0, stream>>>(ctxf, owt, ameta, Ofb);
+    pv_reduce<<<NPAIR, 128, 0, stream>>>(ppart, aga, alist, ctx16);
+    o_mfma<<<dim3(40, 8, EA), 256, 0, stream>>>(ctx16, owt, ameta, Ofb);
     attn_combine<<<NTOK, 256, 0, stream>>>(src, ob, aidx, aga, ainv, Ofb, x1);
 
-    ln_kernel<<<NTOK, 256, 0, stream>>>(x1, ln2_w, ln2_b, xn2);
+    ln_kernel<<<NTOK, 256, 0, stream>>>(x1, ln2_w, ln2_b, xn2, xnb);
     router_kernel<EF><<<NTOK, 64, 0, stream>>>(xn2, fgw, fidx, fga);
     bin_zero<<<1, 64, 0, stream>>>(fmeta);
     bin_count<<<NPAIR / 256, 256, 0, stream>>>(fidx, fmeta);
@@ -801,7 +755,7 @@
     bin_scatter<<<NPAIR / 256, 256, 0, stream>>>(fidx, fmeta, flist, finv);
     convT_kernel<1024, 512><<<dim3(32, 16, EF), 256, 0, stream>>>(w1, w1t);
     convT_kernel<512, 1024><<<dim3(16, 32, EF), 256, 0, stream>>>(w2, w2t);
-    ffn_mfma1<<<dim3(20, 4, EF), 256, 0, stream>>>(xn2, w1t, b1, fmeta, flist, fga, Hb);
+    ffn_mfma1<<<dim3(20, 4, EF), 256, 0, stream>>>(xnb, w1t, b1, fmeta, flist, fga, Hb);
     ffn_mfma2<<<dim3(20, 8, EF), 256, 0, stream>>>(Hb, w2t, fmeta, Of2b);
     ffn_combine<<<NTOK, 256, 0, stream>>>(x1, b2, fidx, fga, finv, Of2b, out);
 }
```

Result: no change. 510.1 us (-1.3%).
